# Kernel tuning notes

Hardware: AMD Instinct MI355X
Metric: run time of the kernel (lower is better)

Reference implementation:

```python
import jax, jax.numpy as jnp
import numpy as np

N_EMBED = 8192
EMBED_DIM = 256
BETA = 0.25


def setup_inputs() -> dict:
    key = jax.random.key(0)
    k1, k2 = jax.random.split(key)
    z = jax.random.normal(k1, (8, 4096, EMBED_DIM), dtype=jnp.float32)
    # original: uniform(-1/n_embed, 1/n_embed)
    embed_weight = jax.random.uniform(
        k2, (N_EMBED, EMBED_DIM), dtype=jnp.float32,
        minval=-1.0 / N_EMBED, maxval=1.0 / N_EMBED)
    return {"z": z, "embed_weight": embed_weight}


def reference(z, embed_weight):
    # z: [B, H, C] with C == embed_dim (no permute needed for this layout)
    B, H, C = z.shape
    z_flat = z.reshape(-1, C)  # [N, C]
    # squared L2 distances: ||z||^2 + ||e||^2 - 2 z e^T  -> [N, n_embed]
    d = (jnp.sum(z_flat * z_flat, axis=1, keepdims=True)
         + jnp.sum(embed_weight * embed_weight, axis=1)
         - 2.0 * jnp.matmul(z_flat, embed_weight.T))
    idx = jnp.argmin(d, axis=1)  # [N]
    z_q = embed_weight[idx].reshape(B, H, C)
    # VQ loss (stop-gradient semantics irrelevant for the forward value)
    loss = (jnp.mean((jax.lax.stop_gradient(z_q) - z) ** 2)
            + BETA * jnp.mean((z_q - jax.lax.stop_gradient(z)) ** 2))
    # straight-through estimator
    z_q_st = z + jax.lax.stop_gradient(z_q - z)
    return (z_q_st, loss, idx.reshape(B, H))
```

## Files before the change

### kernel.cpp

```cpp
#include <hip/hip_runtime.h>
#include <math.h>

#define DIM     256
#define NROWS   32768
#define NCODES  8192
#define ZQ_ELEMS (NROWS * DIM)

#define CAND_MAX 64
#define DELTA    5.0e-4f
#define NCB      4
#define COLS_PER_CB (NCODES / NCB)
#define BM 128
#define BN 64
#define CHUNKS (COLS_PER_CB / BN)
#define LCAP 1984

typedef __attribute__((ext_vector_type(8))) short bf16x8;
typedef __attribute__((ext_vector_type(4))) float f32x4;

__device__ __forceinline__ unsigned short bf16rne(float x) {
    unsigned u = __float_as_uint(x);
    unsigned r = (u + 0x7FFFu + ((u >> 16) & 1u)) >> 16;
    return (unsigned short)r;
}

__device__ __forceinline__ float pw128_sq(const float* __restrict__ a) {
    float r[8];
#pragma unroll
    for (int j = 0; j < 8; ++j) r[j] = __fmul_rn(a[j], a[j]);
#pragma unroll
    for (int i = 8; i < 128; i += 8) {
#pragma unroll
        for (int j = 0; j < 8; ++j) r[j] = __fadd_rn(r[j], __fmul_rn(a[i + j], a[i + j]));
    }
    return __fadd_rn(__fadd_rn(__fadd_rn(r[0], r[1]), __fadd_rn(r[2], r[3])),
                     __fadd_rn(__fadd_rn(r[4], r[5]), __fadd_rn(r[6], r[7])));
}

__global__ __launch_bounds__(256) void rowsq_bf16_kernel(const float* __restrict__ src,
                                                         float* __restrict__ dst,
                                                         unsigned short* __restrict__ bdst) {
    __shared__ float tile[32][DIM + 1];
    const int row0 = blockIdx.x * 32;
    for (int e = threadIdx.x; e < 32 * DIM / 4; e += 256) {
        int r = e >> 6, c4 = e & 63;
        float4 v = *(const float4*)&src[(size_t)(row0 + r) * DIM + c4 * 4];
        tile[r][c4 * 4 + 0] = v.x; tile[r][c4 * 4 + 1] = v.y;
        tile[r][c4 * 4 + 2] = v.z; tile[r][c4 * 4 + 3] = v.w;
        ushort4 o;
        o.x = bf16rne(v.x); o.y = bf16rne(v.y); o.z = bf16rne(v.z); o.w = bf16rne(v.w);
        ((ushort4*)bdst)[(size_t)(row0 + r) * 64 + c4] = o;
    }
    __syncthreads();
    if (threadIdx.x < 32) {
        const float* a = tile[threadIdx.x];
        float s0 = pw128_sq(a);
        float s1 = pw128_sq(a + 128);
        dst[row0 + threadIdx.x] = __fadd_rn(s0, s1);
    }
}

__global__ __launch_bounds__(256) void initbuf_kernel(unsigned long long* __restrict__ keys,
                                                      int* __restrict__ cnt,
                                                      int* __restrict__ flags) {
    int t = blockIdx.x * 256 + threadIdx.x;
    keys[t] = 0xFFFFFFFFFFFFFFFFull;
    cnt[t] = 0;
    flags[t] = 0;
}

__device__ __forceinline__ void gload_lds16(const void* g, void* l) {
    __builtin_amdgcn_global_load_lds(
        (const __attribute__((address_space(1))) unsigned int*)g,
        (__attribute__((address_space(3))) unsigned int*)l, 16, 0, 0);
}

__device__ __forceinline__ void stage32k(const char* gbase, char* lbase,
                                         int wave, int lane) {
#pragma unroll
    for (int it = 0; it < 8; ++it) {
        int ubase = it * 4096 + wave * 1024;
        int loff  = ubase + (lane << 4);
        int goff  = loff ^ (((loff >> 9) & 7) << 4);
        gload_lds16(gbase + goff, lbase + ubase);
    }
}

#define WAIT_VM8()  asm volatile("s_waitcnt vmcnt(8)" ::: "memory")
#define WAIT_VM0()  asm volatile("s_waitcnt vmcnt(0)" ::: "memory")
#define LGKM0()     asm volatile("s_waitcnt lgkmcnt(0)" ::: "memory")
#define SBAR()      __builtin_amdgcn_s_barrier()
#define SCHEDB()    __builtin_amdgcn_sched_barrier(0)

__global__ __launch_bounds__(256, 2) void mfma_filter_kernel(
    const unsigned short* __restrict__ zb, const unsigned short* __restrict__ wb,
    const float* __restrict__ Q,
    int* __restrict__ cnt, int* __restrict__ cand, int* __restrict__ flags) {
    __shared__ __align__(16) unsigned short sbuf[2 * BN * DIM];
    __shared__ __align__(16) float qlds[COLS_PER_CB];
    __shared__ unsigned list[LCAP];
    __shared__ unsigned lcnt;

    const int tid  = threadIdx.x;
    const int wave = tid >> 6;
    const int lane = tid & 63;
    const int l15 = lane & 15, lg = lane >> 4;
    const int bid = blockIdx.x;
    const int r8  = bid & 7;
    const int cb  = r8 >> 1;
    const int rb  = ((bid >> 3) << 1) | (r8 & 1);
    const int row0 = rb * BM;
    const int colbase = cb * COLS_PER_CB;
    const int swz = (l15 & 7) << 4;

    if (tid == 0) lcnt = 0;

    bf16x8 afr[2][8];
    const unsigned short* za = zb + (size_t)(row0 + wave * 32 + l15) * DIM + lg * 8;
#pragma unroll
    for (int fr = 0; fr < 2; ++fr)
#pragma unroll
        for (int kc = 0; kc < 8; ++kc)
            afr[fr][kc] = __builtin_nontemporal_load(
                (const bf16x8*)(za + (size_t)fr * 16 * DIM + kc * 32));
    SCHEDB();

#pragma unroll
    for (int it = 0; it < 2; ++it) {
        int ubase = it * 4096 + wave * 1024;
        gload_lds16((const char*)(Q + colbase) + ubase + (lane << 4),
                    (char*)qlds + ubase);
    }
    stage32k((const char*)(wb + ((size_t)colbase << 8)), (char*)sbuf, wave, lane);
    stage32k((const char*)(wb + ((size_t)(colbase + BN) << 8)),
             (char*)sbuf + 32768, wave, lane);
    LGKM0();
    WAIT_VM8();
    SCHEDB();
    SBAR();
    SCHEDB();

    float rmn[2][4];
#pragma unroll
    for (int fr = 0; fr < 2; ++fr)
#pragma unroll
        for (int j = 0; j < 4; ++j) rmn[fr][j] = INFINITY;

    f32x4 pacc[2][4];

#pragma unroll 1
    for (int ch = 0; ch < CHUNKS; ++ch) {
        const char* bb = (const char*)sbuf + ((ch & 1) << 15);

        f32x4 acc[2][4];
#pragma unroll
        for (int fr = 0; fr < 2; ++fr)
#pragma unroll
            for (int fc = 0; fc < 4; ++fc) acc[fr][fc] = (f32x4){0.f, 0.f, 0.f, 0.f};

#pragma unroll
        for (int kc = 0; kc < 8; ++kc) {
            bf16x8 bfr[4];
#pragma unroll
            for (int fc = 0; fc < 4; ++fc)
                bfr[fc] = *(const bf16x8*)(bb +
                    ((((fc * 16 + l15) << 9) + (kc << 6) + (lg << 4)) ^ swz));
#pragma unroll
            for (int fr = 0; fr < 2; ++fr)
#pragma unroll
                for (int fc = 0; fc < 4; ++fc)
                    acc[fr][fc] = __builtin_amdgcn_mfma_f32_16x16x32_bf16(
                        afr[fr][kc], bfr[fc], acc[fr][fc], 0, 0, 0);
        }

        float qv[4];
#pragma unroll
        for (int fc = 0; fc < 4; ++fc) qv[fc] = qlds[ch * BN + fc * 16 + l15];
#pragma unroll
        for (int fr = 0; fr < 2; ++fr)
#pragma unroll
            for (int fc = 0; fc < 4; ++fc)
#pragma unroll
                for (int j = 0; j < 4; ++j)
                    acc[fr][fc][j] = qv[fc] - 2.0f * acc[fr][fc][j];

#pragma unroll
        for (int fr = 0; fr < 2; ++fr)
#pragma unroll
            for (int j = 0; j < 4; ++j) {
                float mn = fminf(fminf(acc[fr][0][j], acc[fr][1][j]),
                                 fminf(acc[fr][2][j], acc[fr][3][j]));
#pragma unroll
                for (int off = 1; off < 16; off <<= 1)
                    mn = fminf(mn, __shfl_xor(mn, off));
                rmn[fr][j] = fminf(rmn[fr][j], mn);
            }

        LGKM0();
        SCHEDB();
        SBAR();
        SCHEDB();

        if (ch + 2 < CHUNKS)
            stage32k((const char*)(wb + ((size_t)(colbase + (ch + 2) * BN) << 8)),
                     (char*)sbuf + ((ch & 1) << 15), wave, lane);

        if (ch > 0) {
            const int code0 = colbase + (ch - 1) * BN;
#pragma unroll
            for (int fr = 0; fr < 2; ++fr)
#pragma unroll
                for (int j = 0; j < 4; ++j) {
                    float thr = rmn[fr][j] + DELTA;
                    const int rl = wave * 32 + fr * 16 + lg * 4 + j;
#pragma unroll
                    for (int fc = 0; fc < 4; ++fc) {
                        if (pacc[fr][fc][j] <= thr) {
                            int code = code0 + fc * 16 + l15;
                            unsigned s = atomicAdd(&lcnt, 1u);
                            if (s < LCAP) {
                                list[s] = ((unsigned)rl << 13) | (unsigned)code;
                            } else {
                                int row = row0 + rl;
                                int slot = atomicAdd(&cnt[row], 1);
                                if (slot < CAND_MAX)
                                    cand[(size_t)row * CAND_MAX + slot] = code;
                                else flags[row] = 1;
                            }
                        }
                    }
                }
        }
#pragma unroll
        for (int fr = 0; fr < 2; ++fr)
#pragma unroll
            for (int fc = 0; fc < 4; ++fc) pacc[fr][fc] = acc[fr][fc];

        if (ch + 2 < CHUNKS) {
            WAIT_VM8();
        } else {
            WAIT_VM0();
        }
        SCHEDB();
        SBAR();
        SCHEDB();
    }

    {
        const int code0 = colbase + (CHUNKS - 1) * BN;
#pragma unroll
        for (int fr = 0; fr < 2; ++fr)
#pragma unroll
            for (int j = 0; j < 4; ++j) {
                float thr = rmn[fr][j] + DELTA;
                const int rl = wave * 32 + fr * 16 + lg * 4 + j;
#pragma unroll
                for (int fc = 0; fc < 4; ++fc) {
                    if (pacc[fr][fc][j] <= thr) {
                        int code = code0 + fc * 16 + l15;
                        unsigned s = atomicAdd(&lcnt, 1u);
                        if (s < LCAP) {
                            list[s] = ((unsigned)rl << 13) | (unsigned)code;
                        } else {
                            int row = row0 + rl;
                            int slot = atomicAdd(&cnt[row], 1);
                            if (slot < CAND_MAX)
                                cand[(size_t)row * CAND_MAX + slot] = code;
                            else flags[row] = 1;
                        }
                    }
                }
            }
    }

    LGKM0();
    SCHEDB();
    SBAR();
    SCHEDB();
    unsigned n = lcnt;
    if (n > LCAP) n = LCAP;
    for (unsigned i = tid; i < n; i += 256) {
        unsigned e = list[i];
        int rl = (int)(e >> 13);
        int code = (int)(e & 8191u);
        int row = row0 + rl;
        int slot = atomicAdd(&cnt[row], 1);
        if (slot < CAND_MAX) cand[(size_t)row * CAND_MAX + slot] = code;
        else flags[row] = 1;
    }
}

__global__ __launch_bounds__(256) void recheck_kernel(
    const float* __restrict__ z, const float* __restrict__ w,
    const float* __restrict__ P, const float* __restrict__ Q,
    const int* __restrict__ cnt, const int* __restrict__ cand,
    const int* __restrict__ flags, unsigned long long* __restrict__ keys) {
    const int gid  = blockIdx.x * 256 + threadIdx.x;
    const int row  = gid >> 6;
    const int slot = gid & 63;
    const float* zr = z + (size_t)row * DIM;

    if (flags[row]) {
        for (int j = slot; j < NCODES; j += 64) {
            const float* wj = w + (size_t)j * DIM;
            float m = 0.0f;
            for (int k = 0; k < DIM; ++k) m = fmaf(zr[k], wj[k], m);
            float d = __fsub_rn(__fadd_rn(P[row], Q[j]), __fmul_rn(2.0f, m));
            unsigned long long key =
                ((unsigned long long)__float_as_uint(d) << 32) | (unsigned)j;
            atomicMin(&keys[row], key);
        }
        return;
    }
    int n = cnt[row]; if (n > CAND_MAX) n = CAND_MAX;
    if (slot >= n) return;
    const int j = cand[(size_t)row * CAND_MAX + slot];
    const float* wj = w + (size_t)j * DIM;
    float m = 0.0f;
    for (int k = 0; k < DIM; ++k) m = fmaf(zr[k], wj[k], m);
    float d = __fsub_rn(__fadd_rn(P[row], Q[j]), __fmul_rn(2.0f, m));
    unsigned long long key = ((unsigned long long)__float_as_uint(d) << 32) | (unsigned)j;
    atomicMin(&keys[row], key);
}

__global__ __launch_bounds__(256) void finalize_kernel(
    const unsigned long long* __restrict__ keys,
    int* __restrict__ idx_i, float* __restrict__ idx_f) {
    int r = blockIdx.x * 256 + threadIdx.x;
    int j = (int)(unsigned)(keys[r] & 0xFFFFFFFFull);
    idx_i[r] = j;
    idx_f[r] = (float)j;
}

__global__ __launch_bounds__(256) void gather_loss_kernel(
    const float* __restrict__ z, const float* __restrict__ w,
    const int* __restrict__ idx_i, float* __restrict__ zq_out,
    double* __restrict__ partial) {
    __shared__ double red[256];
    const int t    = blockIdx.x * 256 + threadIdx.x;
    const int base = t * 4;
    const int row  = base >> 8;
    const int c    = base & 255;
    const int code = idx_i[row];
    f32x4 zv = __builtin_nontemporal_load((const f32x4*)&z[base]);
    f32x4 wv = *(const f32x4*)&w[(size_t)code * DIM + c];
    float o[4];
    double s = 0.0;
#pragma unroll
    for (int j = 0; j < 4; ++j) {
        float diff = __fsub_rn(wv[j], zv[j]);
        o[j] = __fadd_rn(zv[j], diff);
        double dd = (double)diff;
        s += dd * dd;
    }
    f32x4 ov = { o[0], o[1], o[2], o[3] };
    __builtin_nontemporal_store(ov, (f32x4*)&zq_out[base]);
    red[threadIdx.x] = s;
    __syncthreads();
    for (int st = 128; st > 0; st >>= 1) {
        if (threadIdx.x < st) red[threadIdx.x] += red[threadIdx.x + st];
        __syncthreads();
    }
    if (threadIdx.x == 0) partial[blockIdx.x] = red[0];
}

__global__ __launch_bounds__(256) void loss_final_kernel(const double* __restrict__ partial,
                                                         float* __restrict__ loss_out) {
    __shared__ double red[256];
    double s = 0.0;
    for (int i = threadIdx.x; i < 8192; i += 256) s += partial[i];
    red[threadIdx.x] = s;
    __syncthreads();
    for (int st = 128; st > 0; st >>= 1) {
        if (threadIdx.x < st) red[threadIdx.x] += red[threadIdx.x + st];
        __syncthreads();
    }
    if (threadIdx.x == 0)
        loss_out[0] = (float)(1.25 * red[0] / (double)ZQ_ELEMS);
}

#define FB_BM 128
#define FB_BN 128
#define FB_BK 32
#define FB_PITCH 132

__global__ __launch_bounds__(256, 4) void vq_partial_kernel(
    const float* __restrict__ z, const float* __restrict__ w,
    const float* __restrict__ P, const float* __restrict__ Q,
    float* __restrict__ cand_d, int* __restrict__ cand_i) {
    __shared__ float As[FB_BK][FB_PITCH];
    __shared__ float Bs[FB_BK][FB_PITCH];
    const int tid  = threadIdx.x;
    const int rb   = blockIdx.x >> 2;
    const int cb   = blockIdx.x & 3;
    const int row0 = rb * FB_BM;
    const int colbase = cb * COLS_PER_CB;
    const int rg = tid >> 4;
    const int cg = tid & 15;
    float Pr[8];
#pragma unroll
    for (int i = 0; i < 8; ++i) Pr[i] = P[row0 + rg * 8 + i];
    float bestD[8]; int bestI[8];
#pragma unroll
    for (int i = 0; i < 8; ++i) { bestD[i] = INFINITY; bestI[i] = 0; }
    for (int ct = 0; ct < COLS_PER_CB; ct += FB_BN) {
        const int c0 = colbase + ct;
        float acc[8][8];
#pragma unroll
        for (int i = 0; i < 8; ++i)
#pragma unroll
            for (int j = 0; j < 8; ++j) acc[i][j] = 0.0f;
        for (int kc = 0; kc < DIM; kc += FB_BK) {
            __syncthreads();
#pragma unroll
            for (int it = 0; it < 4; ++it) {
                int u = it * 256 + tid;
                int r = u >> 3, kg = u & 7;
                float4 a = *(const float4*)&z[(size_t)(row0 + r) * DIM + kc + kg * 4];
                As[kg * 4 + 0][r] = a.x; As[kg * 4 + 1][r] = a.y;
                As[kg * 4 + 2][r] = a.z; As[kg * 4 + 3][r] = a.w;
                float4 b = *(const float4*)&w[(size_t)(c0 + r) * DIM + kc + kg * 4];
                Bs[kg * 4 + 0][r] = b.x; Bs[kg * 4 + 1][r] = b.y;
                Bs[kg * 4 + 2][r] = b.z; Bs[kg * 4 + 3][r] = b.w;
            }
            __syncthreads();
#pragma unroll
            for (int k = 0; k < FB_BK; ++k) {
                float av[8], bv[8];
                { float4 t = *(const float4*)&As[k][rg * 8];
                  av[0]=t.x; av[1]=t.y; av[2]=t.z; av[3]=t.w; }
                { float4 t = *(const float4*)&As[k][rg * 8 + 4];
                  av[4]=t.x; av[5]=t.y; av[6]=t.z; av[7]=t.w; }
                { float4 t = *(const float4*)&Bs[k][cg * 4];
                  bv[0]=t.x; bv[1]=t.y; bv[2]=t.z; bv[3]=t.w; }
                { float4 t = *(const float4*)&Bs[k][cg * 4 + 64];
                  bv[4]=t.x; bv[5]=t.y; bv[6]=t.z; bv[7]=t.w; }
#pragma unroll
                for (int i = 0; i < 8; ++i)
#pragma unroll
                    for (int j = 0; j < 8; ++j)
                        acc[i][j] = fmaf(av[i], bv[j], acc[i][j]);
            }
        }
        float qv[8];
        { float4 t = *(const float4*)&Q[c0 + cg * 4];
          qv[0]=t.x; qv[1]=t.y; qv[2]=t.z; qv[3]=t.w; }
        { float4 t = *(const float4*)&Q[c0 + 64 + cg * 4];
          qv[4]=t.x; qv[5]=t.y; qv[6]=t.z; qv[7]=t.w; }
#pragma unroll
        for (int i = 0; i < 8; ++i)
#pragma unroll
            for (int j = 0; j < 8; ++j) {
                float d = __fsub_rn(__fadd_rn(Pr[i], qv[j]), __fmul_rn(2.0f, acc[i][j]));
                int code = c0 + ((j < 4) ? (cg * 4 + j) : (64 + cg * 4 + (j - 4)));
                if (d < bestD[i]) { bestD[i] = d; bestI[i] = code; }
            }
    }
#pragma unroll
    for (int off = 1; off < 16; off <<= 1)
#pragma unroll
        for (int i = 0; i < 8; ++i) {
            float od = __shfl_xor(bestD[i], off);
            int   oi = __shfl_xor(bestI[i], off);
            if (od < bestD[i] || (od == bestD[i] && oi < bestI[i])) {
                bestD[i] = od; bestI[i] = oi;
            }
        }
    if (cg == 0)
#pragma unroll
        for (int i = 0; i < 8; ++i) {
            int row = row0 + rg * 8 + i;
            cand_d[cb * NROWS + row] = bestD[i];
            cand_i[cb * NROWS + row] = bestI[i];
        }
}

__global__ __launch_bounds__(256) void argmin_reduce_kernel(
    const float* __restrict__ cand_d, const int* __restrict__ cand_i,
    int* __restrict__ idx_i, float* __restrict__ idx_f) {
    const int row = blockIdx.x * 256 + threadIdx.x;
    float bd = cand_d[row];
    int   bi = cand_i[row];
#pragma unroll
    for (int cb = 1; cb < NCB; ++cb) {
        float d = cand_d[cb * NROWS + row];
        int   ii = cand_i[cb * NROWS + row];
        if (d < bd || (d == bd && ii < bi)) { bd = d; bi = ii; }
    }
    idx_i[row] = bi;
    idx_f[row] = (float)bi;
}

extern "C" void kernel_launch(void* const* d_in, const int* in_sizes, int n_in,
                              void* d_out, int out_size, void* d_ws, size_t ws_size,
                              hipStream_t stream) {
    const float* z = (const float*)d_in[0];
    const float* w = (const float*)d_in[1];
    float* out = (float*)d_out;

    float* ws = (float*)d_ws;
    unsigned short* zb = (unsigned short*)ws;
    unsigned short* wb = (unsigned short*)(ws + 4194304);
    float*  P       = ws + 4194304 + 1048576;
    float*  Q       = P + NROWS;
    int*    idx_i   = (int*)(Q + NCODES);
    double* partial = (double*)(idx_i + NROWS);
    unsigned long long* keys = (unsigned long long*)(partial + 8192);
    int*    cnt     = (int*)(keys + NROWS);
    int*    flags   = cnt + NROWS;
    int*    cand    = flags + NROWS;
    const size_t NEED = ((size_t)(4194304 + 1048576 + 32768 + 8192 + 32768 + 16384 + 65536
                                  + 32768 + 32768 + 2097152)) * 4;

    if (ws_size >= NEED) {
        rowsq_bf16_kernel<<<NROWS / 32, 256, 0, stream>>>(z, P, zb);
        rowsq_bf16_kernel<<<NCODES / 32, 256, 0, stream>>>(w, Q, wb);
        initbuf_kernel<<<NROWS / 256, 256, 0, stream>>>(keys, cnt, flags);
        mfma_filter_kernel<<<(NROWS / BM) * NCB, 256, 0, stream>>>(zb, wb, Q, cnt, cand, flags);
        recheck_kernel<<<NROWS * CAND_MAX / 256, 256, 0, stream>>>(z, w, P, Q, cnt, cand,
                                                                   flags, keys);
        finalize_kernel<<<NROWS / 256, 256, 0, stream>>>(keys, idx_i, out + ZQ_ELEMS + 1);
    } else {
        rowsq_bf16_kernel<<<NROWS / 32, 256, 0, stream>>>(z, P, zb);
        rowsq_bf16_kernel<<<NCODES / 32, 256, 0, stream>>>(w, Q, wb);
        float* cand_d = (float*)(partial + 8192);
        int*   cand_i = (int*)(cand_d + NCB * NROWS);
        vq_partial_kernel<<<(NROWS / FB_BM) * NCB, 256, 0, stream>>>(z, w, P, Q, cand_d, cand_i);
        argmin_reduce_kernel<<<NROWS / 256, 256, 0, stream>>>(cand_d, cand_i, idx_i,
                                                              out + ZQ_ELEMS + 1);
    }

    gather_loss_kernel<<<ZQ_ELEMS / (256 * 4), 256, 0, stream>>>(z, w, idx_i, out, partial);
    loss_final_kernel<<<1, 256, 0, stream>>>(partial, out + ZQ_ELEMS);
}
```

Before: 528.6 us.

## Move distance epilogue after barrier, use DPP row-min, skip rows early, vectorize recheck

The distance conversion and per-row min reduction now run after the chunk barrier and the next tile's stage issue, so they overlap with global loads. The shuffle-based 16-lane min is replaced with DPP row operations. Each row's local min is kept so rows with no candidate under the threshold skip the per-column checks. The MFMA loop runs at raised wave priority, and the recheck dot product uses float4 loads. Risks include the DPP controls not matching the 16-lane grouping and more register pressure from keeping pmn.

```diff
diff --git a/kernel.cpp b/kernel.cpp
--- a/kernel.cpp
+++ b/kernel.cpp
@@ -22,6 +22,19 @@
     unsigned u = __float_as_uint(x);
     unsigned r = (u + 0x7FFFu + ((u >> 16) & 1u)) >> 16;
     return (unsigned short)r;
+}
+
+template<int CTRL>
+__device__ __forceinline__ float dppmin(float x) {
+    int y = __builtin_amdgcn_update_dpp(0, __float_as_int(x), CTRL, 0xF, 0xF, false);
+    return fminf(x, __int_as_float(y));
+}
+__device__ __forceinline__ float rowmin16(float x) {
+    x = dppmin<0xB1>(x);
+    x = dppmin<0x4E>(x);
+    x = dppmin<0x141>(x);
+    x = dppmin<0x140>(x);
+    return x;
 }
 
 __device__ __forceinline__ float pw128_sq(const float* __restrict__ a) {
@@ -147,6 +160,7 @@
         for (int j = 0; j < 4; ++j) rmn[fr][j] = INFINITY;
 
     f32x4 pacc[2][4];
+    float pmn[2][4];
 
 #pragma unroll 1
     for (int ch = 0; ch < CHUNKS; ++ch) {
@@ -158,6 +172,7 @@
 #pragma unroll
             for (int fc = 0; fc < 4; ++fc) acc[fr][fc] = (f32x4){0.f, 0.f, 0.f, 0.f};
 
+        __builtin_amdgcn_s_setprio(1);
 #pragma unroll
         for (int kc = 0; kc < 8; ++kc) {
             bf16x8 bfr[4];
@@ -172,29 +187,7 @@
                     acc[fr][fc] = __builtin_amdgcn_mfma_f32_16x16x32_bf16(
                         afr[fr][kc], bfr[fc], acc[fr][fc], 0, 0, 0);
         }
-
-        float qv[4];
-#pragma unroll
-        for (int fc = 0; fc < 4; ++fc) qv[fc] = qlds[ch * BN + fc * 16 + l15];
-#pragma unroll
-        for (int fr = 0; fr < 2; ++fr)
-#pragma unroll
-            for (int fc = 0; fc < 4; ++fc)
-#pragma unroll
-                for (int j = 0; j < 4; ++j)
-                    acc[fr][fc][j] = qv[fc] - 2.0f * acc[fr][fc][j];
-
-#pragma unroll
-        for (int fr = 0; fr < 2; ++fr)
-#pragma unroll
-            for (int j = 0; j < 4; ++j) {
-                float mn = fminf(fminf(acc[fr][0][j], acc[fr][1][j]),
-                                 fminf(acc[fr][2][j], acc[fr][3][j]));
-#pragma unroll
-                for (int off = 1; off < 16; off <<= 1)
-                    mn = fminf(mn, __shfl_xor(mn, off));
-                rmn[fr][j] = fminf(rmn[fr][j], mn);
-            }
+        __builtin_amdgcn_s_setprio(0);
 
         LGKM0();
         SCHEDB();
@@ -205,6 +198,27 @@
             stage32k((const char*)(wb + ((size_t)(colbase + (ch + 2) * BN) << 8)),
                      (char*)sbuf + ((ch & 1) << 15), wave, lane);
 
+        float qv[4];
+#pragma unroll
+        for (int fc = 0; fc < 4; ++fc) qv[fc] = qlds[ch * BN + fc * 16 + l15];
+#pragma unroll
+        for (int fr = 0; fr < 2; ++fr)
+#pragma unroll
+            for (int fc = 0; fc < 4; ++fc)
+#pragma unroll
+                for (int j = 0; j < 4; ++j)
+                    acc[fr][fc][j] = qv[fc] - 2.0f * acc[fr][fc][j];
+
+        float lmn[2][4];
+#pragma unroll
+        for (int fr = 0; fr < 2; ++fr)
+#pragma unroll
+            for (int j = 0; j < 4; ++j) {
+                lmn[fr][j] = fminf(fminf(acc[fr][0][j], acc[fr][1][j]),
+                                   fminf(acc[fr][2][j], acc[fr][3][j]));
+                rmn[fr][j] = fminf(rmn[fr][j], rowmin16(lmn[fr][j]));
+            }
+
         if (ch > 0) {
             const int code0 = colbase + (ch - 1) * BN;
 #pragma unroll
@@ -212,6 +226,53 @@
 #pragma unroll
                 for (int j = 0; j < 4; ++j) {
                     float thr = rmn[fr][j] + DELTA;
+                    if (pmn[fr][j] <= thr) {
+                        const int rl = wave * 32 + fr * 16 + lg * 4 + j;
+#pragma unroll
+                        for (int fc = 0; fc < 4; ++fc) {
+                            if (pacc[fr][fc][j] <= thr) {
+                                int code = code0 + fc * 16 + l15;
+                                unsigned s = atomicAdd(&lcnt, 1u);
+                                if (s < LCAP) {
+                                    list[s] = ((unsigned)rl << 13) | (unsigned)code;
+                                } else {
+                                    int row = row0 + rl;
+                                    int slot = atomicAdd(&cnt[row], 1);
+                                    if (slot < CAND_MAX)
+                                        cand[(size_t)row * CAND_MAX + slot] = code;
+                                    else flags[row] = 1;
+                                }
+                            }
+                        }
+                    }
+                }
+        }
+#pragma unroll
+        for (int fr = 0; fr < 2; ++fr) {
+#pragma unroll
+            for (int fc = 0; fc < 4; ++fc) pacc[fr][fc] = acc[fr][fc];
+#pragma unroll
+            for (int j = 0; j < 4; ++j) pmn[fr][j] = lmn[fr][j];
+        }
+
+        if (ch + 2 < CHUNKS) {
+            WAIT_VM8();
+        } else {
+            WAIT_VM0();
+        }
+        SCHEDB();
+        SBAR();
+        SCHEDB();
+    }
+
+    {
+        const int code0 = colbase + (CHUNKS - 1) * BN;
+#pragma unroll
+        for (int fr = 0; fr < 2; ++fr)
+#pragma unroll
+            for (int j = 0; j < 4; ++j) {
+                float thr = rmn[fr][j] + DELTA;
+                if (pmn[fr][j] <= thr) {
                     const int rl = wave * 32 + fr * 16 + lg * 4 + j;
 #pragma unroll
                     for (int fc = 0; fc < 4; ++fc) {
@@ -230,46 +291,6 @@
                         }
                     }
                 }
-        }
-#pragma unroll
-        for (int fr = 0; fr < 2; ++fr)
-#pragma unroll
-            for (int fc = 0; fc < 4; ++fc) pacc[fr][fc] = acc[fr][fc];
-
-        if (ch + 2 < CHUNKS) {
-            WAIT_VM8();
-        } else {
-            WAIT_VM0();
-        }
-        SCHEDB();
-        SBAR();
-        SCHEDB();
-    }
-
-    {
-        const int code0 = colbase + (CHUNKS - 1) * BN;
-#pragma unroll
-        for (int fr = 0; fr < 2; ++fr)
-#pragma unroll
-            for (int j = 0; j < 4; ++j) {
-                float thr = rmn[fr][j] + DELTA;
-                const int rl = wave * 32 + fr * 16 + lg * 4 + j;
-#pragma unroll
-                for (int fc = 0; fc < 4; ++fc) {
-                    if (pacc[fr][fc][j] <= thr) {
-                        int code = code0 + fc * 16 + l15;
-                        unsigned s = atomicAdd(&lcnt, 1u);
-                        if (s < LCAP) {
-                            list[s] = ((unsigned)rl << 13) | (unsigned)code;
-                        } else {
-                            int row = row0 + rl;
-                            int slot = atomicAdd(&cnt[row], 1);
-                            if (slot < CAND_MAX)
-                                cand[(size_t)row * CAND_MAX + slot] = code;
-                            else flags[row] = 1;
-                        }
-                    }
-                }
             }
     }
 
@@ -290,6 +311,22 @@
     }
 }
 
+__device__ __forceinline__ float exact_dot(const float* __restrict__ zr,
+                                           const float* __restrict__ wj) {
+    const f32x4* z4 = (const f32x4*)zr;
+    const f32x4* w4 = (const f32x4*)wj;
+    float m = 0.0f;
+#pragma unroll 8
+    for (int k4 = 0; k4 < 64; ++k4) {
+        f32x4 a = z4[k4], b = w4[k4];
+        m = fmaf(a[0], b[0], m);
+        m = fmaf(a[1], b[1], m);
+        m = fmaf(a[2], b[2], m);
+        m = fmaf(a[3], b[3], m);
+    }
+    return m;
+}
+
 __global__ __launch_bounds__(256) void recheck_kernel(
     const float* __restrict__ z, const float* __restrict__ w,
     const float* __restrict__ P, const float* __restrict__ Q,
@@ -302,9 +339,7 @@
 
     if (flags[row]) {
         for (int j = slot; j < NCODES; j += 64) {
-            const float* wj = w + (size_t)j * DIM;
-            float m = 0.0f;
-            for (int k = 0; k < DIM; ++k) m = fmaf(zr[k], wj[k], m);
+            float m = exact_dot(zr, w + (size_t)j * DIM);
             float d = __fsub_rn(__fadd_rn(P[row], Q[j]), __fmul_rn(2.0f, m));
             unsigned long long key =
                 ((unsigned long long)__float_as_uint(d) << 32) | (unsigned)j;
@@ -315,9 +350,7 @@
     int n = cnt[row]; if (n > CAND_MAX) n = CAND_MAX;
     if (slot >= n) return;
     const int j = cand[(size_t)row * CAND_MAX + slot];
-    const float* wj = w + (size_t)j * DIM;
-    float m = 0.0f;
-    for (int k = 0; k < DIM; ++k) m = fmaf(zr[k], wj[k], m);
+    float m = exact_dot(zr, w + (size_t)j * DIM);
     float d = __fsub_rn(__fadd_rn(P[row], Q[j]), __fmul_rn(2.0f, m));
     unsigned long long key = ((unsigned long long)__float_as_uint(d) << 32) | (unsigned)j;
     atomicMin(&keys[row], key);
```

Result: faster. 489.0 us (-7.5%).
